# Performance work log

Measured on AMD Instinct MI355X. Metric: run time of the kernel, lower is better.

The kernel has to match this reference:

```python
import jax, jax.numpy as jnp
import numpy as np

NUM_EXPERTS = 16
HIDDEN_DIM = 1024
TOP_K = 4
INPUT_DIM = 4096
OUTPUT_DIM = 4096
BATCH = 4096


def setup_inputs() -> dict:
    key = jax.random.key(0)
    ks = jax.random.split(key, 6)
    total_cols = NUM_EXPERTS * HIDDEN_DIM
    return {
        "x": jax.random.normal(ks[0], (BATCH, INPUT_DIM), dtype=jnp.float32),
        "gate_w": jax.random.normal(ks[1], (INPUT_DIM, NUM_EXPERTS), dtype=jnp.float32) * 0.02,
        "gate_b": jnp.zeros((NUM_EXPERTS,), dtype=jnp.float32),
        "weight": jax.random.normal(ks[2], (INPUT_DIM, total_cols), dtype=jnp.float32) * 0.01,
        "agg_w": jax.random.normal(ks[3], (total_cols, OUTPUT_DIM), dtype=jnp.float32) * 0.02,
        "agg_b": jnp.zeros((OUTPUT_DIM,), dtype=jnp.float32),
    }


def reference(x, gate_w, gate_b, weight, agg_w, agg_b):
    # 1) gating logits (batch, E), 2) sum over batch -> (E,)
    gating_logits = x @ gate_w + gate_b
    gating_sum = gating_logits.sum(axis=0)
    # 3) global top-k expert selection -> binary mask over experts
    _, topk_inds = jax.lax.top_k(gating_sum, TOP_K)
    expert_mask = jnp.zeros((NUM_EXPERTS,), dtype=x.dtype).at[topk_inds].set(1.0)
    # 4/5) block-sparse matmul: mask replicated over all row blocks, so each
    # expert's column block [e*H:(e+1)*H] is x @ W_block if selected else 0.
    out_sparse = x @ weight  # (batch, E*H)
    col_mask = jnp.repeat(expert_mask, HIDDEN_DIM)  # (E*H,)
    out_sparse = out_sparse * col_mask[None, :]
    # 6) aggregator
    final_out = out_sparse @ agg_w + agg_b
    return final_out
```

## Files before the change

### kernel.cpp

```cpp
#include <hip/hip_runtime.h>
#include <hip/hip_bf16.h>


#define BATCH 4096
#define DIN 4096
#define NE 16
#define HD 1024
#define TOPK 4
#define TOTC (NE * HD)
#define NT 64

using bf16 = __hip_bfloat16;
typedef __attribute__((ext_vector_type(8))) short short8;
typedef __attribute__((ext_vector_type(4))) float f32x4;

__device__ inline short f2bs(float f) {
  __hip_bfloat16 h = __float2bfloat16(f);
  return *reinterpret_cast<short*>(&h);
}

__global__ void k_cvtsum(const float* __restrict__ x, bf16* __restrict__ xb,
                         float* __restrict__ colsum) {
  const int t = threadIdx.x;
  const int lane = t & 63;
  const int w = t >> 6;
  const int c = blockIdx.x * 256 + lane * 4;
  const int r0 = blockIdx.y * 128 + w * 32;
  float4 s = {0.f, 0.f, 0.f, 0.f};
  for (int i = 0; i < 32; ++i) {
    size_t off = (size_t)(r0 + i) * DIN + c;
    float4 v = *reinterpret_cast<const float4*>(x + off);
    s.x += v.x; s.y += v.y; s.z += v.z; s.w += v.w;
    ushort4 b;
    b.x = (unsigned short)f2bs(v.x); b.y = (unsigned short)f2bs(v.y);
    b.z = (unsigned short)f2bs(v.z); b.w = (unsigned short)f2bs(v.w);
    *reinterpret_cast<ushort4*>(reinterpret_cast<char*>(xb) + off * 2) = b;
  }
  __shared__ float sm[4][256];
  sm[w][lane * 4 + 0] = s.x; sm[w][lane * 4 + 1] = s.y;
  sm[w][lane * 4 + 2] = s.z; sm[w][lane * 4 + 3] = s.w;
  __syncthreads();
  float tot = sm[0][t] + sm[1][t] + sm[2][t] + sm[3][t];
  atomicAdd(&colsum[blockIdx.x * 256 + t], tot);
}

__global__ void k_gate(const float* __restrict__ colsum, const float* __restrict__ gw,
                       const float* __restrict__ gb, int* __restrict__ ids) {
  __shared__ float red[4][16];
  __shared__ float gs[16];
  int t = threadIdx.x;
  int e = t & 15, kg = t >> 4;
  float p = 0.f;
  for (int k = kg; k < DIN; k += 16) p += colsum[k] * gw[(size_t)k * NE + e];
  p += __shfl_down(p, 32);
  p += __shfl_down(p, 16);
  if ((t & 63) < 16) red[t >> 6][e] = p;
  __syncthreads();
  if (t < 16) gs[t] = red[0][t] + red[1][t] + red[2][t] + red[3][t] + (float)BATCH * gb[t];
  __syncthreads();
  if (t == 0) {
    float v[16];
    #pragma unroll
    for (int i = 0; i < 16; ++i) v[i] = gs[i];
    for (int j = 0; j < TOPK; ++j) {
      int bi = 0;
      float bv = v[0];
      for (int i2 = 1; i2 < 16; ++i2)
        if (v[i2] > bv) { bv = v[i2]; bi = i2; }
      ids[j] = bi;
      v[bi] = -3.4e38f;
    }
  }
}

__global__ void k_gather(const float* __restrict__ w, const float* __restrict__ a,
                         const int* __restrict__ ids,
                         bf16* __restrict__ wbt, bf16* __restrict__ abt) {
  __shared__ float tile[64 * 65];
  const int t = threadIdx.x;
  const int tc = t & 15, kr = t >> 4;
  const int tk = t & 7, nr0 = t >> 3;
  for (int tl = blockIdx.x; tl < 8192; tl += 2048) {
    const int wsel = tl < 4096;
    const int tidx = wsel ? tl : tl - 4096;
    const int k0 = (tidx & 63) * 64, n0 = (tidx >> 6) * 64;
    if (wsel) {
      const int e = ids[n0 >> 10];
      const int wc0 = e * HD + (n0 & 1023);
      #pragma unroll
      for (int j = 0; j < 4; ++j) {
        int kk = kr + j * 16;
        float4 v = *reinterpret_cast<const float4*>(w + (size_t)(k0 + kk) * TOTC + wc0 + tc * 4);
        float* dst = &tile[kk * 65 + tc * 4];
        dst[0] = v.x; dst[1] = v.y; dst[2] = v.z; dst[3] = v.w;
      }
    } else {
      const int e = ids[k0 >> 10];
      const int ar0 = e * HD + (k0 & 1023);
      #pragma unroll
      for (int j = 0; j < 4; ++j) {
        int kk = kr + j * 16;
        float4 v = *reinterpret_cast<const float4*>(a + (size_t)(ar0 + kk) * 4096 + n0 + tc * 4);
        float* dst = &tile[kk * 65 + tc * 4];
        dst[0] = v.x; dst[1] = v.y; dst[2] = v.z; dst[3] = v.w;
      }
    }
    __syncthreads();
    bf16* dstp = wsel ? wbt : abt;
    #pragma unroll
    for (int i = 0; i < 2; ++i) {
      int n = n0 + nr0 + i * 32;
      short8 r;
      #pragma unroll
      for (int m = 0; m < 8; ++m) r[m] = f2bs(tile[(tk * 8 + m) * 65 + nr0 + i * 32]);
      *reinterpret_cast<short8*>(dstp + (size_t)n * DIN + k0 + tk * 8) = r;
    }
    __syncthreads();
  }
}

#define MFMA_BF16 __builtin_amdgcn_mfma_f32_16x16x32_bf16
#define VM4 asm volatile("s_waitcnt vmcnt(4)" ::: "memory")
#define VM0 asm volatile("s_waitcnt vmcnt(0)" ::: "memory")
#define NOST ((void)0)
#define NOPREF ((void)0)

#define PH(BUF, Q, BF, STG, GATE, PREF)                                         \
  do {                                                                          \
    short8 aA0 = LDA(BUF, 2 * (Q), 0), aA1 = LDA(BUF, 2 * (Q), 1);              \
    short8 aB0 = LDA(BUF, 2 * (Q) + 1, 0), aB1 = LDA(BUF, 2 * (Q) + 1, 1);      \
    STG;                                                                        \
    GATE;                                                                       \
    __builtin_amdgcn_sched_barrier(0);                                          \
    __builtin_amdgcn_s_barrier();                                               \
    asm volatile("s_waitcnt lgkmcnt(0)" ::: "memory");                          \
    __builtin_amdgcn_sched_barrier(0);                                          \
    PREF;                                                                       \
    __builtin_amdgcn_s_setprio(1);                                              \
    _Pragma("unroll") for (int nf = 0; nf < 4; ++nf) {                          \
      acc[2 * (Q)][nf] = MFMA_BF16(aA0, BF[nf][0], acc[2 * (Q)][nf], 0, 0, 0);          \
      acc[2 * (Q)][nf] = MFMA_BF16(aA1, BF[nf][1], acc[2 * (Q)][nf], 0, 0, 0);          \
      acc[2 * (Q) + 1][nf] = MFMA_BF16(aB0, BF[nf][0], acc[2 * (Q) + 1][nf], 0, 0, 0);  \
      acc[2 * (Q) + 1][nf] = MFMA_BF16(aB1, BF[nf][1], acc[2 * (Q) + 1][nf], 0, 0, 0);  \
    }                                                                           \
    __builtin_amdgcn_s_setprio(0);                                              \
    __builtin_amdgcn_s_barrier();                                               \
  } while (0)

#define PREF_INTO(BF, BUF)                                                      \
  _Pragma("unroll") for (int nf = 0; nf < 4; ++nf) {                            \
    BF[nf][0] = LDB(BUF, nf, 0);                                                \
    BF[nf][1] = LDB(BUF, nf, 1);                                                \
  }

template <int STORE_F32>
__global__ __launch_bounds__(512, 2) void k_gemm8(
    const bf16* __restrict__ A, const bf16* __restrict__ Bt,
    bf16* __restrict__ Cb, float* __restrict__ Cf, const float* __restrict__ bias) {
  __shared__ __align__(16) char smraw[131072];
  const int t = threadIdx.x;
  const int lane = t & 63;
  const int w = t >> 6;
  const int wr = w >> 2;
  const int wc = w & 3;

  const int bid = blockIdx.x;
  const int xcd = bid & 7;
  const int i = bid >> 3;
  const int bm = ((xcd >> 1) * 4 + (i & 3)) * 256;
  const int bn = ((xcd & 1) * 8 + (i >> 2)) * 256;

  f32x4 acc[8][4] = {};
  short8 bfragE[4][2];
  short8 bfragO[4][2];

  const int srow = w * 16 + (lane >> 3);
  const int sgr = lane & 7;

  auto STAGE_A = [&](int buf, int half, int kt) {
    char* lb = smraw + buf * 65536 + half * 16384 + w * 2048 + lane * 16;
    #pragma unroll
    for (int i2 = 0; i2 < 2; ++i2) {
      int r = srow + i2 * 8;
      const bf16* g = A + (size_t)(bm + half * 128 + r) * 4096 + kt * 64 + ((sgr ^ (r & 7)) * 8);
      __builtin_amdgcn_global_load_lds(
          (const __attribute__((address_space(1))) void*)g,
          (__attribute__((address_space(3))) void*)(lb + i2 * 1024), 16, 0, 0);
    }
  };
  auto STAGE_B = [&](int buf, int half, int kt) {
    char* lb = smraw + buf * 65536 + 32768 + half * 16384 + w * 2048 + lane * 16;
    #pragma unroll
    for (int i2 = 0; i2 < 2; ++i2) {
      int r = srow + i2 * 8;
      const bf16* g = Bt + (size_t)(bn + half * 128 + r) * 4096 + kt * 64 + ((sgr ^ (r & 7)) * 8);
      __builtin_amdgcn_global_load_lds(
          (const __attribute__((address_space(1))) void*)g,
          (__attribute__((address_space(3))) void*)(lb + i2 * 1024), 16, 0, 0);
    }
  };
  auto LDA = [&](int buf, int mf, int kk) -> short8 {
    int r = mf * 16 + (lane & 15);
    int kb = ((kk * 4 + (lane >> 4)) ^ (r & 7)) * 16;
    return *reinterpret_cast<const short8*>(smraw + buf * 65536 + wr * 16384 + r * 128 + kb);
  };
  auto LDB = [&](int buf, int nf, int kk) -> short8 {
    int nc = wc * 64 + nf * 16 + (lane & 15);
    int half = nc >> 7, r = nc & 127;
    int kb = ((kk * 4 + (lane >> 4)) ^ (r & 7)) * 16;
    return *reinterpret_cast<const short8*>(smraw + buf * 65536 + 32768 + half * 16384 + r * 128 + kb);
  };

  STAGE_B(0, 0, 0); STAGE_B(0, 1, 0);
  STAGE_A(0, 0, 0); STAGE_A(0, 1, 0);
  STAGE_B(1, 0, 1); STAGE_B(1, 1, 1);
  VM4;
  __builtin_amdgcn_s_barrier();
  PREF_INTO(bfragE, 0)

  for (int tt = 0; tt < 31; ++tt) {
    const int a = 2 * tt;
    PH(0, 0, bfragE, STAGE_A(1, 0, a + 1), NOST, NOPREF);
    PH(0, 1, bfragE, STAGE_A(1, 1, a + 1), NOST, NOPREF);
    PH(0, 2, bfragE, STAGE_B(0, 0, a + 2), NOST, NOPREF);
    PH(0, 3, bfragE, STAGE_B(0, 1, a + 2), VM4, PREF_INTO(bfragO, 1));
    PH(1, 0, bfragO, STAGE_A(0, 0, a + 2), NOST, NOPREF);
    PH(1, 1, bfragO, STAGE_A(0, 1, a + 2), NOST, NOPREF);
    PH(1, 2, bfragO, STAGE_B(1, 0, a + 3), NOST, NOPREF);
    PH(1, 3, bfragO, STAGE_B(1, 1, a + 3), VM4, PREF_INTO(bfragE, 0));
  }
  PH(0, 0, bfragE, STAGE_A(1, 0, 63), NOST, NOPREF);
  PH(0, 1, bfragE, STAGE_A(1, 1, 63), NOST, NOPREF);
  PH(0, 2, bfragE, NOST, NOST, NOPREF);
  PH(0, 3, bfragE, NOST, VM0, PREF_INTO(bfragO, 1));
  PH(1, 0, bfragO, NOST, NOST, NOPREF);
  PH(1, 1, bfragO, NOST, NOST, NOPREF);
  PH(1, 2, bfragO, NOST, NOST, NOPREF);
  PH(1, 3, bfragO, NOST, NOST, NOPREF);

  const int cr = (lane >> 4) * 4;
  const int cc = lane & 15;
  #pragma unroll
  for (int mf = 0; mf < 8; ++mf) {
    #pragma unroll
    for (int nf = 0; nf < 4; ++nf) {
      int row = bm + wr * 128 + mf * 16 + cr;
      int col = bn + wc * 64 + nf * 16 + cc;
      #pragma unroll
      for (int r = 0; r < 4; ++r) {
        if constexpr (STORE_F32) {
          Cf[(size_t)(row + r) * 4096 + col] = acc[mf][nf][r] + bias[col];
        } else {
          Cb[(size_t)(row + r) * 4096 + col] = __float2bfloat16(acc[mf][nf][r]);
        }
      }
    }
  }
}

extern "C" void kernel_launch(void* const* d_in, const int* in_sizes, int n_in,
                              void* d_out, int out_size, void* d_ws, size_t ws_size,
                              hipStream_t stream) {
  const float* x = (const float*)d_in[0];
  const float* gate_w = (const float*)d_in[1];
  const float* gate_b = (const float*)d_in[2];
  const float* weight = (const float*)d_in[3];
  const float* agg_w = (const float*)d_in[4];
  const float* agg_b = (const float*)d_in[5];
  float* out = (float*)d_out;
  char* ws = (char*)d_ws;

  float* colsum = (float*)ws;
  int* ids = (int*)(ws + 16384);
  bf16* mid = (bf16*)(ws + (4u << 20));
  bf16* abt = (bf16*)(ws + (36u << 20));
  bf16* xb = (bf16*)d_out;
  bf16* wbt = (bf16*)((char*)d_out + (32u << 20));

  hipMemsetAsync(colsum, 0, DIN * sizeof(float), stream);
  k_cvtsum<<<dim3(16, 32), 256, 0, stream>>>(x, xb, colsum);
  k_gate<<<1, 256, 0, stream>>>(colsum, gate_w, gate_b, ids);
  k_gather<<<2048, 256, 0, stream>>>(weight, agg_w, ids, wbt, abt);
  k_gemm8<0><<<256, 512, 0, stream>>>(xb, wbt, mid, nullptr, nullptr);
  k_gemm8<1><<<256, 512, 0, stream>>>(mid, abt, nullptr, out, agg_b);
}
```

Before: 387.1 us.

## Retile bf16 GEMMs to 128x256 blocks with K=32 triple-buffered LDS pipeline

```diff
diff --git a/kernel.cpp b/kernel.cpp
--- a/kernel.cpp
+++ b/kernel.cpp
@@ -8,7 +8,6 @@
 #define HD 1024
 #define TOPK 4
 #define TOTC (NE * HD)
-#define NT 64
 
 using bf16 = __hip_bfloat16;
 typedef __attribute__((ext_vector_type(8))) short short8;
@@ -120,44 +119,46 @@
 }
 
 #define MFMA_BF16 __builtin_amdgcn_mfma_f32_16x16x32_bf16
-#define VM4 asm volatile("s_waitcnt vmcnt(4)" ::: "memory")
+#define VM3 asm volatile("s_waitcnt vmcnt(3)" ::: "memory")
 #define VM0 asm volatile("s_waitcnt vmcnt(0)" ::: "memory")
 #define NOST ((void)0)
-#define NOPREF ((void)0)
-
-#define PH(BUF, Q, BF, STG, GATE, PREF)                                         \
+
+#define ITER(BC, STG, GATE)                                                     \
   do {                                                                          \
-    short8 aA0 = LDA(BUF, 2 * (Q), 0), aA1 = LDA(BUF, 2 * (Q), 1);              \
-    short8 aB0 = LDA(BUF, 2 * (Q) + 1, 0), aB1 = LDA(BUF, 2 * (Q) + 1, 1);      \
+    short8 af0 = LDA(BC, 0), af1 = LDA(BC, 1), af2 = LDA(BC, 2), af3 = LDA(BC, 3); \
+    short8 bf0 = LDB(BC, 0), bf1 = LDB(BC, 1), bf2 = LDB(BC, 2), bf3 = LDB(BC, 3); \
     STG;                                                                        \
     GATE;                                                                       \
     __builtin_amdgcn_sched_barrier(0);                                          \
     __builtin_amdgcn_s_barrier();                                               \
     asm volatile("s_waitcnt lgkmcnt(0)" ::: "memory");                          \
     __builtin_amdgcn_sched_barrier(0);                                          \
-    PREF;                                                                       \
     __builtin_amdgcn_s_setprio(1);                                              \
-    _Pragma("unroll") for (int nf = 0; nf < 4; ++nf) {                          \
-      acc[2 * (Q)][nf] = MFMA_BF16(aA0, BF[nf][0], acc[2 * (Q)][nf], 0, 0, 0);          \
-      acc[2 * (Q)][nf] = MFMA_BF16(aA1, BF[nf][1], acc[2 * (Q)][nf], 0, 0, 0);          \
-      acc[2 * (Q) + 1][nf] = MFMA_BF16(aB0, BF[nf][0], acc[2 * (Q) + 1][nf], 0, 0, 0);  \
-      acc[2 * (Q) + 1][nf] = MFMA_BF16(aB1, BF[nf][1], acc[2 * (Q) + 1][nf], 0, 0, 0);  \
-    }                                                                           \
+    acc[0][0] = MFMA_BF16(af0, bf0, acc[0][0], 0, 0, 0);                        \
+    acc[0][1] = MFMA_BF16(af0, bf1, acc[0][1], 0, 0, 0);                        \
+    acc[0][2] = MFMA_BF16(af0, bf2, acc[0][2], 0, 0, 0);                        \
+    acc[0][3] = MFMA_BF16(af0, bf3, acc[0][3], 0, 0, 0);                        \
+    acc[1][0] = MFMA_BF16(af1, bf0, acc[1][0], 0, 0, 0);                        \
+    acc[1][1] = MFMA_BF16(af1, bf1, acc[1][1], 0, 0, 0);                        \
+    acc[1][2] = MFMA_BF16(af1, bf2, acc[1][2], 0, 0, 0);                        \
+    acc[1][3] = MFMA_BF16(af1, bf3, acc[1][3], 0, 0, 0);                        \
+    acc[2][0] = MFMA_BF16(af2, bf0, acc[2][0], 0, 0, 0);                        \
+    acc[2][1] = MFMA_BF16(af2, bf1, acc[2][1], 0, 0, 0);                        \
+    acc[2][2] = MFMA_BF16(af2, bf2, acc[2][2], 0, 0, 0);                        \
+    acc[2][3] = MFMA_BF16(af2, bf3, acc[2][3], 0, 0, 0);                        \
+    acc[3][0] = MFMA_BF16(af3, bf0, acc[3][0], 0, 0, 0);                        \
+    acc[3][1] = MFMA_BF16(af3, bf1, acc[3][1], 0, 0, 0);                        \
+    acc[3][2] = MFMA_BF16(af3, bf2, acc[3][2], 0, 0, 0);                        \
+    acc[3][3] = MFMA_BF16(af3, bf3, acc[3][3], 0, 0, 0);                        \
     __builtin_amdgcn_s_setprio(0);                                              \
     __builtin_amdgcn_s_barrier();                                               \
   } while (0)
 
-#define PREF_INTO(BF, BUF)                                                      \
-  _Pragma("unroll") for (int nf = 0; nf < 4; ++nf) {                            \
-    BF[nf][0] = LDB(BUF, nf, 0);                                                \
-    BF[nf][1] = LDB(BUF, nf, 1);                                                \
-  }
-
 template <int STORE_F32>
-__global__ __launch_bounds__(512, 2) void k_gemm8(
+__global__ __launch_bounds__(512, 4) void k_gemm3(
     const bf16* __restrict__ A, const bf16* __restrict__ Bt,
     bf16* __restrict__ Cb, float* __restrict__ Cf, const float* __restrict__ bias) {
-  __shared__ __align__(16) char smraw[131072];
+  __shared__ __align__(16) char smraw[73728];
   const int t = threadIdx.x;
   const int lane = t & 63;
   const int w = t >> 6;
@@ -167,84 +168,60 @@
   const int bid = blockIdx.x;
   const int xcd = bid & 7;
   const int i = bid >> 3;
-  const int bm = ((xcd >> 1) * 4 + (i & 3)) * 256;
-  const int bn = ((xcd & 1) * 8 + (i >> 2)) * 256;
-
-  f32x4 acc[8][4] = {};
-  short8 bfragE[4][2];
-  short8 bfragO[4][2];
-
-  const int srow = w * 16 + (lane >> 3);
-  const int sgr = lane & 7;
-
-  auto STAGE_A = [&](int buf, int half, int kt) {
-    char* lb = smraw + buf * 65536 + half * 16384 + w * 2048 + lane * 16;
-    #pragma unroll
-    for (int i2 = 0; i2 < 2; ++i2) {
-      int r = srow + i2 * 8;
-      const bf16* g = A + (size_t)(bm + half * 128 + r) * 4096 + kt * 64 + ((sgr ^ (r & 7)) * 8);
+  const int bm = ((xcd & 3) * 8 + (i & 7)) * 128;
+  const int bn = ((xcd >> 2) * 8 + (i >> 3)) * 256;
+
+  f32x4 acc[4][4] = {};
+
+  const int sr = w * 16 + (lane >> 2);
+  const int sc = ((lane & 3) ^ (sr & 3)) * 8;
+
+  auto STAGE = [&](int buf, int kt) {
+    char* lb = smraw + buf * 24576 + w * 1024 + lane * 16;
+    const bf16* ga = A + (size_t)(bm + sr) * 4096 + kt * 32 + sc;
+    __builtin_amdgcn_global_load_lds(
+        (const __attribute__((address_space(1))) void*)ga,
+        (__attribute__((address_space(3))) void*)lb, 16, 0, 0);
+    #pragma unroll
+    for (int p = 0; p < 2; ++p) {
+      const bf16* gb = Bt + (size_t)(bn + sr + p * 128) * 4096 + kt * 32 + sc;
       __builtin_amdgcn_global_load_lds(
-          (const __attribute__((address_space(1))) void*)g,
-          (__attribute__((address_space(3))) void*)(lb + i2 * 1024), 16, 0, 0);
+          (const __attribute__((address_space(1))) void*)gb,
+          (__attribute__((address_space(3))) void*)(lb + 8192 + p * 8192), 16, 0, 0);
     }
   };
-  auto STAGE_B = [&](int buf, int half, int kt) {
-    char* lb = smraw + buf * 65536 + 32768 + half * 16384 + w * 2048 + lane * 16;
-    #pragma unroll
-    for (int i2 = 0; i2 < 2; ++i2) {
-      int r = srow + i2 * 8;
-      const bf16* g = Bt + (size_t)(bn + half * 128 + r) * 4096 + kt * 64 + ((sgr ^ (r & 7)) * 8);
-      __builtin_amdgcn_global_load_lds(
-          (const __attribute__((address_space(1))) void*)g,
-          (__attribute__((address_space(3))) void*)(lb + i2 * 1024), 16, 0, 0);
-    }
+  auto LDA = [&](int buf, int mf) -> short8 {
+    int r = wr * 64 + mf * 16 + (lane & 15);
+    int g = (lane >> 4) ^ (r & 3);
+    return *reinterpret_cast<const short8*>(smraw + buf * 24576 + r * 64 + g * 16);
   };
-  auto LDA = [&](int buf, int mf, int kk) -> short8 {
-    int r = mf * 16 + (lane & 15);
-    int kb = ((kk * 4 + (lane >> 4)) ^ (r & 7)) * 16;
-    return *reinterpret_cast<const short8*>(smraw + buf * 65536 + wr * 16384 + r * 128 + kb);
+  auto LDB = [&](int buf, int nf) -> short8 {
+    int r = wc * 64 + nf * 16 + (lane & 15);
+    int g = (lane >> 4) ^ (r & 3);
+    return *reinterpret_cast<const short8*>(smraw + buf * 24576 + 8192 + r * 64 + g * 16);
   };
-  auto LDB = [&](int buf, int nf, int kk) -> short8 {
-    int nc = wc * 64 + nf * 16 + (lane & 15);
-    int half = nc >> 7, r = nc & 127;
-    int kb = ((kk * 4 + (lane >> 4)) ^ (r & 7)) * 16;
-    return *reinterpret_cast<const short8*>(smraw + buf * 65536 + 32768 + half * 16384 + r * 128 + kb);
-  };
-
-  STAGE_B(0, 0, 0); STAGE_B(0, 1, 0);
-  STAGE_A(0, 0, 0); STAGE_A(0, 1, 0);
-  STAGE_B(1, 0, 1); STAGE_B(1, 1, 1);
-  VM4;
+
+  STAGE(0, 0);
+  STAGE(1, 1);
+  VM3;
   __builtin_amdgcn_s_barrier();
-  PREF_INTO(bfragE, 0)
-
-  for (int tt = 0; tt < 31; ++tt) {
-    const int a = 2 * tt;
-    PH(0, 0, bfragE, STAGE_A(1, 0, a + 1), NOST, NOPREF);
-    PH(0, 1, bfragE, STAGE_A(1, 1, a + 1), NOST, NOPREF);
-    PH(0, 2, bfragE, STAGE_B(0, 0, a + 2), NOST, NOPREF);
-    PH(0, 3, bfragE, STAGE_B(0, 1, a + 2), VM4, PREF_INTO(bfragO, 1));
-    PH(1, 0, bfragO, STAGE_A(0, 0, a + 2), NOST, NOPREF);
-    PH(1, 1, bfragO, STAGE_A(0, 1, a + 2), NOST, NOPREF);
-    PH(1, 2, bfragO, STAGE_B(1, 0, a + 3), NOST, NOPREF);
-    PH(1, 3, bfragO, STAGE_B(1, 1, a + 3), VM4, PREF_INTO(bfragE, 0));
-  }
-  PH(0, 0, bfragE, STAGE_A(1, 0, 63), NOST, NOPREF);
-  PH(0, 1, bfragE, STAGE_A(1, 1, 63), NOST, NOPREF);
-  PH(0, 2, bfragE, NOST, NOST, NOPREF);
-  PH(0, 3, bfragE, NOST, VM0, PREF_INTO(bfragO, 1));
-  PH(1, 0, bfragO, NOST, NOST, NOPREF);
-  PH(1, 1, bfragO, NOST, NOST, NOPREF);
-  PH(1, 2, bfragO, NOST, NOST, NOPREF);
-  PH(1, 3, bfragO, NOST, NOST, NOPREF);
+
+  for (int g3 = 0; g3 < 42; ++g3) {
+    const int a = g3 * 3;
+    ITER(0, STAGE(2, a + 2), VM3);
+    ITER(1, STAGE(0, a + 3), VM3);
+    ITER(2, STAGE(1, a + 4), VM3);
+  }
+  ITER(0, NOST, VM0);
+  ITER(1, NOST, NOST);
 
   const int cr = (lane >> 4) * 4;
   const int cc = lane & 15;
   #pragma unroll
-  for (int mf = 0; mf < 8; ++mf) {
+  for (int mf = 0; mf < 4; ++mf) {
     #pragma unroll
     for (int nf = 0; nf < 4; ++nf) {
-      int row = bm + wr * 128 + mf * 16 + cr;
+      int row = bm + wr * 64 + mf * 16 + cr;
       int col = bn + wc * 64 + nf * 16 + cc;
       #pragma unroll
       for (int r = 0; r < 4; ++r) {
@@ -281,6 +258,6 @@
   k_cvtsum<<<dim3(16, 32), 256, 0, stream>>>(x, xb, colsum);
   k_gate<<<1, 256, 0, stream>>>(colsum, gate_w, gate_b, ids);
   k_gather<<<2048, 256, 0, stream>>>(weight, agg_w, ids, wbt, abt);
-  k_gemm8<0><<<256, 512, 0, stream>>>(xb, wbt, mid, nullptr, nullptr);
-  k_gemm8<1><<<256, 512, 0, stream>>>(mid, abt, nullptr, out, agg_b);
-}
+  k_gemm3<0><<<512, 512, 0, stream>>>(xb, wbt, mid, nullptr, nullptr);
+  k_gemm3<1><<<512, 512, 0, stream>>>(mid, abt, nullptr, out, agg_b);
+}
```

Result: slower. 427.2 us (+10.4%).
